# Kernel optimization log

Measured on AMD Instinct MI355X. Metric: run time of the kernel, lower is better.

## Reference

```python
import jax, jax.numpy as jnp
import numpy as np

N = 256   # events in the document
D = 768   # embed_dim
R = 7     # out_dim == num_relations (label 6 == NONE, filtered from graph)
H = 150   # Score hidden_dim


def _pair_idx(n):
    # torch ordering: [(i,k) for i in range(n) for k in range(n) if i != k]
    ii = np.repeat(np.arange(n), n)
    jj = np.tile(np.arange(n), n)
    m = ii != jj
    return jnp.asarray(ii[m], jnp.int32), jnp.asarray(jj[m], jnp.int32)


def _mlp(x, w1, b1, w2, b2, w3, b3):
    # Score module, eval mode (dropout off)
    h = jax.nn.relu(x @ w1 + b1)
    h = jax.nn.relu(h @ w2 + b2)
    return h @ w3 + b3


def _rgcn_conv(x, src, dst, etype, keep, w, root, bias):
    # PyG RGCNConv (num_bases=None, aggr='mean'):
    # out[i] = sum_r mean_{j in N_r(i)} x_j @ W_r + x_i @ root + bias
    # Linearity lets us aggregate x_j first, then apply W_r once per (node, rel).
    n, d = x.shape
    r = w.shape[0]
    seg = dst.astype(jnp.int32) * r + etype.astype(jnp.int32)      # [E]
    msg = x[src] * keep[:, None]                                   # [E, D]
    agg = jax.ops.segment_sum(msg, seg, num_segments=n * r)        # [N*R, D]
    cnt = jax.ops.segment_sum(keep, seg, num_segments=n * r)       # [N*R]
    mean = (agg / jnp.maximum(cnt, 1.0)[:, None]).reshape(n, r, d)
    return jnp.einsum('nrd,rde->ne', mean, w) + x @ root + bias


def setup_inputs():
    key = jax.random.key(0)
    ks = jax.random.split(key, 12)
    g = lambda k, s, sc=0.02: jax.random.normal(k, s, dtype=jnp.float32) * sc
    P = N * (N - 1)
    z = lambda s: jnp.zeros(s, jnp.float32)
    return {
        'embed': jax.random.normal(ks[0], (N, D), dtype=jnp.float32),
        'labels': jax.random.randint(ks[1], (P,), 0, R),
        'conv1_w': g(ks[2], (R, D, D)), 'conv1_root': g(ks[3], (D, D)), 'conv1_bias': z((D,)),
        'conv2_w': g(ks[4], (R, D, D)), 'conv2_root': g(ks[5], (D, D)), 'conv2_bias': z((D,)),
        'base_w1': g(ks[6], (2 * D, H)), 'base_b1': z((H,)),
        'base_w2': g(ks[7], (H, H)), 'base_b2': z((H,)),
        'base_w3': g(ks[8], (H, R)), 'base_b3': z((R,)),
        'cls_w1': g(ks[9], (2 * D, H)), 'cls_b1': z((H,)),
        'cls_w2': g(ks[10], (H, H)), 'cls_b2': z((H,)),
        'cls_w3': g(ks[11], (H, R)), 'cls_b3': z((R,)),
    }


def reference(embed, labels, conv1_w, conv1_root, conv1_bias,
              conv2_w, conv2_root, conv2_bias,
              base_w1, base_b1, base_w2, base_b2, base_w3, base_b3,
              cls_w1, cls_b1, cls_w2, cls_b2, cls_w3, cls_b3):
    n = embed.shape[0]
    src, dst = _pair_idx(n)                                        # all ordered pairs i != k

    # baseline scorer on raw-embedding pairs (frozen in torch; its argmax is unused)
    pairs0 = jnp.concatenate([embed[src], embed[dst]], axis=1)     # [P, 2D]
    _noise = _mlp(pairs0, base_w1, base_b1, base_w2, base_b2, base_w3, base_b3)

    # graph edges: keep only pairs whose label != 6 (NONE)
    keep = (labels != R - 1).astype(embed.dtype)                   # [P]
    etype = jnp.where(labels == R - 1, 0, labels)                  # dummy type, zero-weighted

    # RGCN (eval mode: dropout off)
    x = jax.nn.relu(_rgcn_conv(embed, src, dst, etype, keep, conv1_w, conv1_root, conv1_bias))
    out = _rgcn_conv(x, src, dst, etype, keep, conv2_w, conv2_root, conv2_bias)

    # classifier on RGCN-output pairs (full pair set again)
    pairs = jnp.concatenate([out[src], out[dst]], axis=1)          # [P, 2D]
    return _mlp(pairs, cls_w1, cls_b1, cls_w2, cls_b2, cls_w3, cls_b3)  # [P, 7]
```

## Files before the change

kernel.cpp:

```cpp
#include <hip/hip_runtime.h>

typedef unsigned short u16;
typedef unsigned int   u32;
typedef __attribute__((ext_vector_type(8))) short bf16x8;
typedef __attribute__((ext_vector_type(4))) float f32x4;

#define KCAT 5376

struct Params {
    const float* embed; const int* labels;
    const float* c1w; const float* c1root; const float* c1b;
    const float* c2w; const float* c2root; const float* c2b;
    const float* cw1; const float* cb1; const float* cw2;
    const float* cb2; const float* cw3; const float* cb3;
    u16* S; float* recip; u16* Acat1; u16* Acat2;
    u16* Pemb; u16* Px; u16* PW1; u16* PC1; u16* Pw2c; u16* Pw3;
    u16* W2C1p; u16* PA2; float* cvec; float* AB; float* outp;
};

__device__ inline u16 f2bf(float f) {
    union { float f; u32 u; } v; v.f = f;
    u32 r = v.u + 0x7FFFu + ((v.u >> 16) & 1u);
    return (u16)(r >> 16);
}
__device__ inline f32x4 mfma16(bf16x8 a, bf16x8 b, f32x4 c) {
    return __builtin_amdgcn_mfma_f32_16x16x32_bf16(a, b, c, 0, 0, 0);
}

__device__ inline void pack_f32(const float* __restrict__ src, int ld, int rows, int cols,
                                u16* __restrict__ dst, int ntot, int kt0, int nt0,
                                int ntiles, int tile) {
    int ktile = tile / ntiles, ntile = tile % ntiles;
    int lane = threadIdx.x & 63;
    int m = lane & 15, hi = lane >> 4;
    int n = ntile * 16 + m;
    u16 tmp[8];
#pragma unroll
    for (int j = 0; j < 8; ++j) {
        int kk = ktile * 32 + hi * 8 + j;
        tmp[j] = (kk < rows && n < cols) ? f2bf(src[(size_t)kk * ld + n]) : (u16)0;
    }
    u16* d = dst + (((size_t)(kt0 + ktile) * ntot + (nt0 + ntile)) * 64 + lane) * 8;
    *(bf16x8*)d = *(const bf16x8*)tmp;
}

__device__ inline void pack_a_f32(const float* __restrict__ src, int ld,
                                  u16* __restrict__ dst, int mt0, int tile) {
    int mtile = tile / 24, ktile = tile % 24;
    int lane = threadIdx.x & 63;
    int m = lane & 15, hi = lane >> 4;
    const float* s = src + (size_t)(mtile * 16 + m) * ld + ktile * 32 + hi * 8;
    f32x4 x0 = *(const f32x4*)(s);
    f32x4 x1 = *(const f32x4*)(s + 4);
    u16 tmp[8];
#pragma unroll
    for (int e = 0; e < 4; ++e) { tmp[e] = f2bf(x0[e]); tmp[e + 4] = f2bf(x1[e]); }
    *(bf16x8*)(dst + (((size_t)(mt0 + mtile) * 24 + ktile) * 64 + lane) * 8) = *(const bf16x8*)tmp;
}

__device__ inline f32x4 gemm_tile(const u16* __restrict__ A, int lda,
                                  const u16* __restrict__ Bp,
                                  int row0, int nt, int ntot, int ktiles) {
    int lane = threadIdx.x & 63;
    int m = lane & 15, hi = lane >> 4;
    const u16* arow = A + (size_t)(row0 + m) * lda + hi * 8;
    const u16* bptr = Bp + ((size_t)nt * 64 + lane) * 8;
    f32x4 acc = {0.f, 0.f, 0.f, 0.f};
#pragma unroll 4
    for (int kt = 0; kt < ktiles; ++kt) {
        bf16x8 a = *(const bf16x8*)(arow + kt * 32);
        bf16x8 b = *(const bf16x8*)(bptr + (size_t)kt * ntot * 512);
        acc = mfma16(a, b, acc);
    }
    return acc;
}

__global__ __launch_bounds__(256) void kp0(Params p) {
    int w = threadIdx.x >> 6, lane = threadIdx.x & 63;
    int job = blockIdx.x * 4 + w;
    if (job < 256) {
        int k = job;
        int lab[4];
#pragma unroll
        for (int g = 0; g < 4; ++g) {
            int i = lane + g * 64;
            lab[g] = (i == k) ? -1 : p.labels[i * 255 + k - (k > i ? 1 : 0)];
        }
#pragma unroll
        for (int r = 0; r < 6; ++r) {
            int c = 0;
#pragma unroll
            for (int g = 0; g < 4; ++g) c += __popcll(__ballot(lab[g] == r));
#pragma unroll
            for (int g = 0; g < 4; ++g) {
                int i = lane + g * 64;
                p.S[(k * 6 + r) * 256 + i] = (lab[g] == r) ? (u16)0x3F80 : (u16)0;
            }
            if (lane == 0) p.recip[k * 6 + r] = 1.0f / (float)(c > 1 ? c : 1);
        }
    } else if (job < 640) {
        int idx = (job - 256) * 512 + lane * 8;
        int row = idx / 768, col = idx - row * 768;
        f32x4 a = *(const f32x4*)(p.embed + idx);
        f32x4 b = *(const f32x4*)(p.embed + idx + 4);
        u16 tmp[8];
#pragma unroll
        for (int e = 0; e < 4; ++e) { tmp[e] = f2bf(a[e]); tmp[e + 4] = f2bf(b[e]); }
        *(bf16x8*)(p.Acat1 + (size_t)row * KCAT + 4608 + col) = *(const bf16x8*)tmp;
    }
    else if (job < 1024) pack_f32(p.embed, 768, 256, 768, p.Pemb, 48, 0, 0, 48, job - 640);
    else if (job < 7936) pack_f32(p.c1w, 768, 4608, 768, p.PW1, 48, 0, 0, 48, job - 1024);
    else if (job < 9088) pack_f32(p.c1root, 768, 768, 768, p.PW1, 48, 144, 0, 48, job - 7936);
    else if (job < 9328) pack_f32(p.cw1, 150, 768, 150, p.PC1, 20, 0, 0, 10, job - 9088);
    else if (job < 9568) pack_f32(p.cw1 + 768 * 150, 150, 768, 150, p.PC1, 20, 0, 10, 10, job - 9328);
    else if (job < 9618) pack_f32(p.cw2, 150, 150, 150, p.Pw2c, 10, 0, 0, 10, job - 9568);
    else if (job < 9623) pack_f32(p.cw3, 7, 150, 7, p.Pw3, 1, 0, 0, 1, job - 9618);
}

__device__ void mean_tile(const Params& p, const u16* Bp, u16* Acat, int tile) {
    int rt = tile / 48, nt = tile % 48;
    f32x4 acc = gemm_tile(p.S, 256, Bp, rt * 16, nt, 48, 8);
    int lane = threadIdx.x & 63;
    int col = nt * 16 + (lane & 15), hi = lane >> 4;
#pragma unroll
    for (int r = 0; r < 4; ++r) {
        int g = rt * 16 + hi * 4 + r;
        float scale = p.recip[g];
        int node = g / 6, rel = g - node * 6;
        Acat[(size_t)node * KCAT + rel * 768 + col] = f2bf(acc[r] * scale);
    }
}

__device__ void w2c1_job(const Params& p, int q) {
    int lane = threadIdx.x & 63;
    int mtb = q / 5, ntb = q % 5;
    int m = lane & 15, hi = lane >> 4;
    f32x4 acc[2][4];
#pragma unroll
    for (int t = 0; t < 2; ++t)
#pragma unroll
        for (int qq = 0; qq < 4; ++qq) acc[t][qq] = {0.f, 0.f, 0.f, 0.f};
    const u16* pa0 = p.PA2 + (((size_t)(mtb * 2)     * 24) * 64 + lane) * 8;
    const u16* pa1 = p.PA2 + (((size_t)(mtb * 2 + 1) * 24) * 64 + lane) * 8;
#pragma unroll 4
    for (int kt = 0; kt < 24; ++kt) {
        bf16x8 a0 = *(const bf16x8*)(pa0 + (size_t)kt * 512);
        bf16x8 a1 = *(const bf16x8*)(pa1 + (size_t)kt * 512);
#pragma unroll
        for (int qq = 0; qq < 4; ++qq) {
            int nt = ntb * 4 + qq;
            bf16x8 b = *(const bf16x8*)(p.PC1 + ((size_t)(kt * 20 + nt) * 64 + lane) * 8);
            acc[0][qq] = mfma16(a0, b, acc[0][qq]);
            acc[1][qq] = mfma16(a1, b, acc[1][qq]);
        }
    }
    int row0 = mtb * 32;
#pragma unroll
    for (int t = 0; t < 2; ++t)
#pragma unroll
        for (int qq = 0; qq < 4; ++qq) {
            int nt = ntb * 4 + qq;
#pragma unroll
            for (int r4 = 0; r4 < 4; ++r4) {
                int kg = row0 + t * 16 + hi * 4 + r4;
                int kt2 = kg >> 5, j = kg & 7, hi2 = (kg >> 3) & 3;
                p.W2C1p[(((size_t)kt2 * 20 + nt) * 64 + hi2 * 16 + m) * 8 + j] = f2bf(acc[t][qq][r4]);
            }
        }
}

__device__ void cvec_job(const Params& p, int nt) {
    int lane = threadIdx.x & 63;
    int m = lane & 15, hi = lane >> 4;
    f32x4 acc = {0.f, 0.f, 0.f, 0.f};
    for (int kt = 0; kt < 24; ++kt) {
        int e0 = kt * 32 + hi * 8;
        f32x4 x0 = *(const f32x4*)(p.c2b + e0);
        f32x4 x1 = *(const f32x4*)(p.c2b + e0 + 4);
        u16 tmp[8];
#pragma unroll
        for (int e = 0; e < 4; ++e) {
            tmp[e]     = (m == 0) ? f2bf(x0[e]) : (u16)0;
            tmp[e + 4] = (m == 0) ? f2bf(x1[e]) : (u16)0;
        }
        bf16x8 a = *(const bf16x8*)tmp;
        bf16x8 b = *(const bf16x8*)(p.PC1 + ((size_t)(kt * 20 + nt) * 64 + lane) * 8);
        acc = mfma16(a, b, acc);
    }
    if (lane < 16) {
        int j = nt * 16 + lane;
        float bias = (j < 150) ? p.cb1[j] : 0.f;
        p.cvec[j] = acc[0] + bias;
    }
}

__global__ __launch_bounds__(256) void kp1(Params p) {
    int w = threadIdx.x >> 6;
    int job = blockIdx.x * 4 + w;
    if (job < 4608)       mean_tile(p, p.Pemb, p.Acat1, job);
    else if (job < 11520) pack_a_f32(p.c2w, 768, p.PA2, 0, job - 4608);
    else if (job < 12672) pack_a_f32(p.c2root, 768, p.PA2, 288, job - 11520);
}

__global__ __launch_bounds__(256) void kp2(Params p) {
    __shared__ float red[4 * 64 * 4];
    int w = threadIdx.x >> 6, lane = threadIdx.x & 63;
    int b = blockIdx.x;
    if (b >= 768) {
        int job = (b - 768) * 4 + w;
        if (job < 840)      w2c1_job(p, job);
        else if (job < 860) cvec_job(p, job - 840);
        return;
    }
    int m = lane & 15, hi = lane >> 4;
    int rt = b / 48, nt = b % 48;
    const u16* arow = p.Acat1 + (size_t)(rt * 16 + m) * KCAT + hi * 8;
    const u16* bptr = p.PW1 + ((size_t)nt * 64 + lane) * 8;
    f32x4 acc = {0.f, 0.f, 0.f, 0.f};
#pragma unroll 4
    for (int kt = w * 42; kt < (w + 1) * 42; ++kt) {
        bf16x8 a = *(const bf16x8*)(arow + kt * 32);
        bf16x8 bb = *(const bf16x8*)(bptr + (size_t)kt * 48 * 512);
        acc = mfma16(a, bb, acc);
    }
    *(f32x4*)&red[(w * 64 + lane) * 4] = acc;
    __syncthreads();
    if (w == 0) {
        f32x4 s = *(f32x4*)&red[lane * 4];
#pragma unroll
        for (int ww = 1; ww < 4; ++ww) s += *(f32x4*)&red[(ww * 64 + lane) * 4];
        int col = nt * 16 + m;
        float bbv = p.c1b[col];
#pragma unroll
        for (int r = 0; r < 4; ++r) {
            int g = rt * 16 + hi * 4 + r;
            float v = fmaxf(s[r] + bbv, 0.f);
            u16 bv = f2bf(v);
            p.Acat2[(size_t)g * KCAT + 4608 + col] = bv;
            p.Px[(((size_t)(g >> 5) * 48 + nt) * 64 + (((g >> 3) & 3) * 16 + m)) * 8 + (g & 7)] = bv;
        }
    }
}

__global__ __launch_bounds__(256) void kp3(Params p) {
    int w = threadIdx.x >> 6;
    int job = blockIdx.x * 4 + w;
    if (job < 4608) mean_tile(p, p.Px, p.Acat2, job);
}

__global__ __launch_bounds__(256) void kp4(Params p) {
    __shared__ float red2[4 * 64 * 4];
    int w = threadIdx.x >> 6, lane = threadIdx.x & 63;
    int m = lane & 15, hi = lane >> 4;
    int b = blockIdx.x;
    int rt = b / 20, nt = b % 20;
    const u16* arow = p.Acat2 + (size_t)(rt * 16 + m) * KCAT + hi * 8;
    const u16* bptr = p.W2C1p + ((size_t)nt * 64 + lane) * 8;
    f32x4 acc = {0.f, 0.f, 0.f, 0.f};
#pragma unroll 4
    for (int kt = w * 42; kt < (w + 1) * 42; ++kt) {
        bf16x8 a = *(const bf16x8*)(arow + kt * 32);
        bf16x8 bb = *(const bf16x8*)(bptr + (size_t)kt * 20 * 512);
        acc = mfma16(a, bb, acc);
    }
    *(f32x4*)&red2[(w * 64 + lane) * 4] = acc;
    __syncthreads();
    if (w == 0) {
        f32x4 s = *(f32x4*)&red2[lane * 4];
#pragma unroll
        for (int ww = 1; ww < 4; ++ww) s += *(f32x4*)&red2[(ww * 64 + lane) * 4];
        int j = nt * 16 + m;
        float cv = p.cvec[j];
#pragma unroll
        for (int r = 0; r < 4; ++r) {
            int g = rt * 16 + hi * 4 + r;
            p.AB[(size_t)g * 320 + j] = s[r] + cv;
        }
    }
}

__global__ __launch_bounds__(256) void kp5(Params p) {
    __shared__ u16 h2t[4][16][168];
    int w = threadIdx.x >> 6, lane = threadIdx.x & 63;
    int m = lane & 15, hi = lane >> 4;
    int pb = blockIdx.x * 64 + w * 16;
    int pp = pb + m;
    int i = pp / 255, rem = pp - i * 255;
    int k = rem + (rem >= i ? 1 : 0);
    const float* Ar = p.AB + (size_t)i * 320;
    const float* Br = p.AB + (size_t)k * 320 + 160;

    bf16x8 af[5];
#pragma unroll
    for (int kk = 0; kk < 5; ++kk) {
        int c = kk * 32 + hi * 8;
        f32x4 a0 = *(const f32x4*)(Ar + c);
        f32x4 a1 = *(const f32x4*)(Ar + c + 4);
        f32x4 b0 = *(const f32x4*)(Br + c);
        f32x4 b1v = *(const f32x4*)(Br + c + 4);
        f32x4 s0 = a0 + b0, s1 = a1 + b1v;
        bf16x8 f;
#pragma unroll
        for (int e = 0; e < 4; ++e) {
            f[e]     = (short)f2bf(fmaxf(s0[e], 0.f));
            f[e + 4] = (short)f2bf(fmaxf(s1[e], 0.f));
        }
        af[kk] = f;
    }

#pragma unroll
    for (int nt = 0; nt < 10; ++nt) {
        f32x4 acc = {0.f, 0.f, 0.f, 0.f};
#pragma unroll
        for (int kk = 0; kk < 5; ++kk) {
            bf16x8 b = *(const bf16x8*)(p.Pw2c + ((size_t)(kk * 10 + nt) * 64 + lane) * 8);
            acc = mfma16(af[kk], b, acc);
        }
        int col = nt * 16 + m;
        float bb = (col < 150) ? p.cb2[col] : 0.f;
#pragma unroll
        for (int r = 0; r < 4; ++r) {
            float v = fmaxf(acc[r] + bb, 0.f);
            h2t[w][hi * 4 + r][col] = f2bf(v);
        }
    }
    __syncthreads();

    f32x4 acc3 = {0.f, 0.f, 0.f, 0.f};
#pragma unroll
    for (int kk = 0; kk < 5; ++kk) {
        bf16x8 a = *(const bf16x8*)(&h2t[w][m][kk * 32 + hi * 8]);
        bf16x8 b = *(const bf16x8*)(p.Pw3 + ((size_t)kk * 64 + lane) * 8);
        acc3 = mfma16(a, b, acc3);
    }
    if (m < 7) {
        float bb = p.cb3[m];
#pragma unroll
        for (int r = 0; r < 4; ++r) {
            int p2 = pb + hi * 4 + r;
            p.outp[p2 * 7 + m] = acc3[r] + bb;
        }
    }
}

extern "C" void kernel_launch(void* const* d_in, const int* in_sizes, int n_in,
                              void* d_out, int out_size, void* d_ws, size_t ws_size,
                              hipStream_t stream) {
    char* ws = (char*)d_ws;
    Params hp;
    hp.embed  = (const float*)d_in[0];
    hp.labels = (const int*)d_in[1];
    hp.c1w    = (const float*)d_in[2];
    hp.c1root = (const float*)d_in[3];
    hp.c1b    = (const float*)d_in[4];
    hp.c2w    = (const float*)d_in[5];
    hp.c2root = (const float*)d_in[6];
    hp.c2b    = (const float*)d_in[7];
    hp.cw1    = (const float*)d_in[14];
    hp.cb1    = (const float*)d_in[15];
    hp.cw2    = (const float*)d_in[16];
    hp.cb2    = (const float*)d_in[17];
    hp.cw3    = (const float*)d_in[18];
    hp.cb3    = (const float*)d_in[19];
    hp.S      = (u16*)(ws + 0);
    hp.recip  = (float*)(ws + 786432);
    hp.Acat1  = (u16*)(ws + 792576);
    hp.Acat2  = (u16*)(ws + 3545088);
    hp.Pemb   = (u16*)(ws + 6297600);
    hp.Px     = (u16*)(ws + 6690816);
    hp.PW1    = (u16*)(ws + 7084032);
    hp.PC1    = (u16*)(ws + 15341568);
    hp.Pw2c   = (u16*)(ws + 15833088);
    hp.Pw3    = (u16*)(ws + 15935488);
    hp.W2C1p  = (u16*)(ws + 15945728);
    hp.cvec   = (float*)(ws + 19386368);
    hp.AB     = (float*)(ws + 19387648);
    hp.PA2    = (u16*)(ws + 19715328);
    hp.outp   = (float*)d_out;

    kp0<<<2406, 256, 0, stream>>>(hp);
    kp1<<<3168, 256, 0, stream>>>(hp);
    kp2<<<983, 256, 0, stream>>>(hp);
    kp3<<<1152, 256, 0, stream>>>(hp);
    kp4<<<320, 256, 0, stream>>>(hp);
    kp5<<<1020, 256, 0, stream>>>(hp);
}
```

Baseline: 92.85 us.

## Compute layer-1 mean aggregation directly from labels and merge into first kernel

The first-layer neighbour mean is now computed per (node, relation) by ballot masks over labels and summing fp32 embedding rows directly, instead of packing embed and running a selection-matrix MFMA GEMM in a separate kernel. The c2w/root packing and the mean jobs move into kp0, which removes one kernel launch and the Pemb buffer. The cost is a data-dependent serial loop per wave with scattered row loads. S and recip are still produced in kp0 for layer 2.

```diff
diff --git a/kernel.cpp b/kernel.cpp
--- a/kernel.cpp
+++ b/kernel.cpp
@@ -3,6 +3,7 @@
 typedef unsigned short u16;
 typedef unsigned int   u32;
 typedef __attribute__((ext_vector_type(8))) short bf16x8;
+typedef __attribute__((ext_vector_type(4))) short u16x4;
 typedef __attribute__((ext_vector_type(4))) float f32x4;
 
 #define KCAT 5376
@@ -14,7 +15,7 @@
     const float* cw1; const float* cb1; const float* cw2;
     const float* cb2; const float* cw3; const float* cb3;
     u16* S; float* recip; u16* Acat1; u16* Acat2;
-    u16* Pemb; u16* Px; u16* PW1; u16* PC1; u16* Pw2c; u16* Pw3;
+    u16* Px; u16* PW1; u16* PC1; u16* Pw2c; u16* Pw3;
     u16* W2C1p; u16* PA2; float* cvec; float* AB; float* outp;
 };
 
@@ -75,6 +76,50 @@
     return acc;
 }
 
+__device__ void mean1_direct(const Params& p, int q) {
+    int k = q / 6, r = q - (q / 6) * 6;
+    int lane = threadIdx.x & 63;
+    int lab[4];
+#pragma unroll
+    for (int g = 0; g < 4; ++g) {
+        int i = lane + g * 64;
+        lab[g] = (i == k) ? -1 : p.labels[i * 255 + k - (k > i ? 1 : 0)];
+    }
+    unsigned long long mask[4];
+    int cnt = 0;
+#pragma unroll
+    for (int g = 0; g < 4; ++g) {
+        mask[g] = __ballot(lab[g] == r);
+        cnt += __popcll(mask[g]);
+    }
+    float scale = 1.0f / (float)(cnt > 1 ? cnt : 1);
+    f32x4 a0 = {0.f,0.f,0.f,0.f}, a1 = {0.f,0.f,0.f,0.f}, a2 = {0.f,0.f,0.f,0.f};
+    const float* ebase = p.embed + lane * 12;
+#pragma unroll
+    for (int g = 0; g < 4; ++g) {
+        unsigned long long mm = mask[g];
+        while (mm) {
+            int b = (int)__builtin_ctzll(mm);
+            mm &= mm - 1;
+            const float* row = ebase + (size_t)(g * 64 + b) * 768;
+            a0 += *(const f32x4*)(row);
+            a1 += *(const f32x4*)(row + 4);
+            a2 += *(const f32x4*)(row + 8);
+        }
+    }
+    u16 tmp[12];
+#pragma unroll
+    for (int e = 0; e < 4; ++e) {
+        tmp[e]     = f2bf(a0[e] * scale);
+        tmp[e + 4] = f2bf(a1[e] * scale);
+        tmp[e + 8] = f2bf(a2[e] * scale);
+    }
+    u16* dst = p.Acat1 + (size_t)k * KCAT + r * 768 + lane * 12;
+    *(u16x4*)(dst)     = *(const u16x4*)(tmp);
+    *(u16x4*)(dst + 4) = *(const u16x4*)(tmp + 4);
+    *(u16x4*)(dst + 8) = *(const u16x4*)(tmp + 8);
+}
+
 __global__ __launch_bounds__(256) void kp0(Params p) {
     int w = threadIdx.x >> 6, lane = threadIdx.x & 63;
     int job = blockIdx.x * 4 + w;
@@ -108,13 +153,15 @@
         for (int e = 0; e < 4; ++e) { tmp[e] = f2bf(a[e]); tmp[e + 4] = f2bf(b[e]); }
         *(bf16x8*)(p.Acat1 + (size_t)row * KCAT + 4608 + col) = *(const bf16x8*)tmp;
     }
-    else if (job < 1024) pack_f32(p.embed, 768, 256, 768, p.Pemb, 48, 0, 0, 48, job - 640);
-    else if (job < 7936) pack_f32(p.c1w, 768, 4608, 768, p.PW1, 48, 0, 0, 48, job - 1024);
-    else if (job < 9088) pack_f32(p.c1root, 768, 768, 768, p.PW1, 48, 144, 0, 48, job - 7936);
-    else if (job < 9328) pack_f32(p.cw1, 150, 768, 150, p.PC1, 20, 0, 0, 10, job - 9088);
-    else if (job < 9568) pack_f32(p.cw1 + 768 * 150, 150, 768, 150, p.PC1, 20, 0, 10, 10, job - 9328);
-    else if (job < 9618) pack_f32(p.cw2, 150, 150, 150, p.Pw2c, 10, 0, 0, 10, job - 9568);
-    else if (job < 9623) pack_f32(p.cw3, 7, 150, 7, p.Pw3, 1, 0, 0, 1, job - 9618);
+    else if (job < 7552)  pack_f32(p.c1w, 768, 4608, 768, p.PW1, 48, 0, 0, 48, job - 640);
+    else if (job < 8704)  pack_f32(p.c1root, 768, 768, 768, p.PW1, 48, 144, 0, 48, job - 7552);
+    else if (job < 8944)  pack_f32(p.cw1, 150, 768, 150, p.PC1, 20, 0, 0, 10, job - 8704);
+    else if (job < 9184)  pack_f32(p.cw1 + 768 * 150, 150, 768, 150, p.PC1, 20, 0, 10, 10, job - 8944);
+    else if (job < 9234)  pack_f32(p.cw2, 150, 150, 150, p.Pw2c, 10, 0, 0, 10, job - 9184);
+    else if (job < 9239)  pack_f32(p.cw3, 7, 150, 7, p.Pw3, 1, 0, 0, 1, job - 9234);
+    else if (job < 16151) pack_a_f32(p.c2w, 768, p.PA2, 0, job - 9239);
+    else if (job < 17303) pack_a_f32(p.c2root, 768, p.PA2, 288, job - 16151);
+    else if (job < 18839) mean1_direct(p, job - 17303);
 }
 
 __device__ void mean_tile(const Params& p, const u16* Bp, u16* Acat, int tile) {
@@ -192,14 +239,6 @@
         float bias = (j < 150) ? p.cb1[j] : 0.f;
         p.cvec[j] = acc[0] + bias;
     }
-}
-
-__global__ __launch_bounds__(256) void kp1(Params p) {
-    int w = threadIdx.x >> 6;
-    int job = blockIdx.x * 4 + w;
-    if (job < 4608)       mean_tile(p, p.Pemb, p.Acat1, job);
-    else if (job < 11520) pack_a_f32(p.c2w, 768, p.PA2, 0, job - 4608);
-    else if (job < 12672) pack_a_f32(p.c2root, 768, p.PA2, 288, job - 11520);
 }
 
 __global__ __launch_bounds__(256) void kp2(Params p) {
@@ -366,7 +405,6 @@
     hp.recip  = (float*)(ws + 786432);
     hp.Acat1  = (u16*)(ws + 792576);
     hp.Acat2  = (u16*)(ws + 3545088);
-    hp.Pemb   = (u16*)(ws + 6297600);
     hp.Px     = (u16*)(ws + 6690816);
     hp.PW1    = (u16*)(ws + 7084032);
     hp.PC1    = (u16*)(ws + 15341568);
@@ -378,8 +416,7 @@
     hp.PA2    = (u16*)(ws + 19715328);
     hp.outp   = (float*)d_out;
 
-    kp0<<<2406, 256, 0, stream>>>(hp);
-    kp1<<<3168, 256, 0, stream>>>(hp);
+    kp0<<<4710, 256, 0, stream>>>(hp);
     kp2<<<983, 256, 0, stream>>>(hp);
     kp3<<<1152, 256, 0, stream>>>(hp);
     kp4<<<320, 256, 0, stream>>>(hp);
```

New measurement: 102.0 us. 1.1x slower.
